# Optimization experiments

Hardware: AMD Instinct MI355X
Metric: run time of the kernel (lower is better)

## Reference

```python
import jax, jax.numpy as jnp
import numpy as np
import math

B, S, D = 16, 1024, 2048  # batch, seq_len, feats_size; LSTM hidden H = D
H = D

def setup_inputs() -> dict:
    key = jax.random.key(0)
    ks = jax.random.split(key, 12)
    s = 1.0 / math.sqrt(D)
    return {
        "feats": jax.random.normal(ks[0], (B, S, D), jnp.float32),
        "Wq": jax.random.normal(ks[1], (D, D), jnp.float32) * s,
        "bq": jnp.zeros((D,), jnp.float32),
        "Wk": jax.random.normal(ks[2], (D, D), jnp.float32) * s,
        "bk": jnp.zeros((D,), jnp.float32),
        "Wv": jax.random.normal(ks[3], (D, D), jnp.float32) * s,
        "bv": jnp.zeros((D,), jnp.float32),
        "W_ih": jax.random.normal(ks[4], (4 * H, D), jnp.float32) * s,
        "W_hh": jax.random.normal(ks[5], (4 * H, H), jnp.float32) * s,
        "b_ih": jnp.zeros((4 * H,), jnp.float32),
        "b_hh": jnp.zeros((4 * H,), jnp.float32),
    }

def _lstm(x, W_ih, W_hh, b_ih, b_hh):
    # x: [B, S, D] -> hidden sequence [B, S, H]. torch nn.LSTM gate order i,f,g,o.
    xg = jnp.einsum('bsd,gd->bsg', x, W_ih) + b_ih + b_hh  # [B,S,4H], input part precomputed
    xg = jnp.swapaxes(xg, 0, 1)  # [S,B,4H] for scan over time
    h0 = jnp.zeros((x.shape[0], H), x.dtype)
    c0 = jnp.zeros((x.shape[0], H), x.dtype)
    def step(carry, xt):
        h, c = carry
        gates = xt + h @ W_hh.T  # [B,4H]
        i, f, g, o = jnp.split(gates, 4, axis=-1)
        c = jax.nn.sigmoid(f) * c + jax.nn.sigmoid(i) * jnp.tanh(g)
        h = jax.nn.sigmoid(o) * jnp.tanh(c)
        return (h, c), h
    _, hs = jax.lax.scan(step, (h0, c0), xg)
    return jnp.swapaxes(hs, 0, 1)  # [B,S,H]

def reference(feats, Wq, bq, Wk, bk, Wv, bv, W_ih, W_hh, b_ih, b_hh):
    q = feats @ Wq.T + bq
    k = feats @ Wk.T + bk
    v = feats @ Wv.T + bv
    dot = jnp.einsum('bsd,btd->bst', q, k) / math.sqrt(2048.0)
    w = jax.nn.softmax(dot, axis=-1)
    new_feats = jnp.einsum('bst,btd->bsd', w, v)
    return _lstm(new_feats, W_ih, W_hh, b_ih, b_hh)
```

## Files before the change

### kernel.cpp

```cpp
#include <hip/hip_runtime.h>


typedef unsigned short u16;
typedef unsigned long long u64;
typedef __attribute__((ext_vector_type(8))) __bf16 bf16x8;
typedef __attribute__((ext_vector_type(8))) unsigned short u16x8;
typedef __attribute__((ext_vector_type(4))) float f32x4;

#define DEV static __device__ __forceinline__

DEV u16 f2bf(float f) {
  union { float f; unsigned u; } x; x.f = f;
  return (u16)((x.u + 0x7FFFu + ((x.u >> 16) & 1u)) >> 16);
}
DEV float bf2f(u16 h) {
  union { unsigned u; float f; } x; x.u = (unsigned)h << 16;
  return x.f;
}
DEV void gload_lds16(const void* g, void* l) {
  __builtin_amdgcn_global_load_lds(
      (const __attribute__((address_space(1))) unsigned int*)g,
      (__attribute__((address_space(3))) unsigned int*)l, 16, 0, 0);
}

__global__ __launch_bounds__(256) void k_cvt(const float* __restrict__ in,
                                             u16* __restrict__ out, long n) {
  long i = (((long)blockIdx.x << 8) | threadIdx.x) << 3;
  if (i >= n) return;
  float4 f0 = *(const float4*)(in + i);
  float4 f1 = *(const float4*)(in + i + 4);
  u16x8 p;
  p[0] = f2bf(f0.x); p[1] = f2bf(f0.y); p[2] = f2bf(f0.z); p[3] = f2bf(f0.w);
  p[4] = f2bf(f1.x); p[5] = f2bf(f1.y); p[6] = f2bf(f1.z); p[7] = f2bf(f1.w);
  *(u16x8*)(out + i) = p;
}

__global__ __launch_bounds__(256) void k_addb(const float* __restrict__ a,
                                              const float* __restrict__ b,
                                              float* __restrict__ o, int n) {
  int i = blockIdx.x * 256 + threadIdx.x;
  if (i < n) o[i] = a[i] + b[i];
}

template<int OBF>
__global__ __launch_bounds__(256) void k_gemm_nt(
    const u16* __restrict__ A, const u16* __restrict__ B, void* __restrict__ Cv,
    const float* __restrict__ bias, float scale, int M, int N, int K,
    long sA, long sB, long sC) {
  __shared__ __attribute__((aligned(16))) u16 As[4096];
  __shared__ __attribute__((aligned(16))) u16 Bs[4096];
  const int tid = threadIdx.x;
  const int lane = tid & 63;
  const int wm = ((tid >> 7) & 1) * 64;
  const int wn = ((tid >> 6) & 1) * 64;
  const int gx = gridDim.x;
  int lin = blockIdx.y * gx + blockIdx.x;
  const int nwg = gx * gridDim.y;
  if ((nwg & 7) == 0) lin = (lin & 7) * (nwg >> 3) + (lin >> 3);
  const long bm = (long)(lin / gx) << 7;
  const long bn = (long)(lin % gx) << 7;
  const u16* Ab = A + (long)blockIdx.z * sA;
  const u16* Bb = B + (long)blockIdx.z * sB;
  const int srow = tid >> 2, scol = (tid & 3) << 3;
  const u16* ga0 = Ab + (bm + srow) * (long)K + scol;
  const u16* gb0 = Bb + (bn + srow) * (long)K + scol;
  const long k64 = (long)K << 6;
  char* lA = (char*)As + tid * 16;
  char* lB = (char*)Bs + tid * 16;
  f32x4 acc[4][4] = {};
  const int fr = lane & 15, fk = (lane >> 4) << 3;
  for (int kt = 0; kt < K; kt += 32) {
    gload_lds16(ga0 + kt, lA);
    gload_lds16(ga0 + k64 + kt, lA + 4096);
    gload_lds16(gb0 + kt, lB);
    gload_lds16(gb0 + k64 + kt, lB + 4096);
    __syncthreads();
    bf16x8 av[4], bv[4];
#pragma unroll
    for (int x = 0; x < 4; ++x) {
      av[x] = *(const bf16x8*)&As[(wm + x * 16 + fr) * 32 + fk];
      bv[x] = *(const bf16x8*)&Bs[(wn + x * 16 + fr) * 32 + fk];
    }
#pragma unroll
    for (int i = 0; i < 4; ++i)
#pragma unroll
      for (int j = 0; j < 4; ++j)
        acc[i][j] = __builtin_amdgcn_mfma_f32_16x16x32_bf16(av[i], bv[j], acc[i][j], 0, 0, 0);
    __syncthreads();
  }
  const long cb = (long)blockIdx.z * sC;
#pragma unroll
  for (int j = 0; j < 4; ++j) {
    const long col = bn + wn + j * 16 + fr;
    const float bb = bias ? bias[col] : 0.f;
#pragma unroll
    for (int i = 0; i < 4; ++i) {
      const long r0 = bm + wm + i * 16 + ((lane >> 4) << 2);
#pragma unroll
      for (int r = 0; r < 4; ++r) {
        const float v = acc[i][j][r] * scale + bb;
        const long off = cb + (r0 + r) * (long)N + col;
        if (OBF) ((u16*)Cv)[off] = f2bf(v);
        else     ((float*)Cv)[off] = v;
      }
    }
  }
}

__global__ __launch_bounds__(256) void k_softmax(const float* __restrict__ S,
                                                 u16* __restrict__ P) {
  __shared__ float red[8];
  const long row = blockIdx.x;
  const float* sr = S + (row << 10);
  const int t = threadIdx.x, lane = t & 63, w = t >> 6;
  float v0 = sr[t], v1 = sr[t + 256], v2 = sr[t + 512], v3 = sr[t + 768];
  float m = fmaxf(fmaxf(v0, v1), fmaxf(v2, v3));
#pragma unroll
  for (int o = 32; o; o >>= 1) m = fmaxf(m, __shfl_xor(m, o));
  if (lane == 0) red[w] = m;
  __syncthreads();
  m = fmaxf(fmaxf(red[0], red[1]), fmaxf(red[2], red[3]));
  v0 = __expf(v0 - m); v1 = __expf(v1 - m); v2 = __expf(v2 - m); v3 = __expf(v3 - m);
  float s = v0 + v1 + v2 + v3;
#pragma unroll
  for (int o = 32; o; o >>= 1) s += __shfl_xor(s, o);
  if (lane == 0) red[4 + w] = s;
  __syncthreads();
  s = red[4] + red[5] + red[6] + red[7];
  const float rs = 1.f / s;
  u16* pr = P + (row << 10);
  pr[t] = f2bf(v0 * rs); pr[t + 256] = f2bf(v1 * rs);
  pr[t + 512] = f2bf(v2 * rs); pr[t + 768] = f2bf(v3 * rs);
}

__global__ __launch_bounds__(256) void k_transpose(const u16* __restrict__ V,
                                                   u16* __restrict__ VT) {
  __shared__ __attribute__((aligned(16))) u16 tile[64][80];
  const long b = blockIdx.z;
  const long t0 = (long)blockIdx.y << 6, d0 = (long)blockIdx.x << 6;
  const int r = threadIdx.x >> 3, c8 = (threadIdx.x & 7) << 3;
  const u16* src = V + ((b << 10) + t0) * 2048 + d0;
#pragma unroll
  for (int p = 0; p < 2; ++p) {
    const int rr = r + p * 32;
    *(u16x8*)&tile[rr][c8] = *(const u16x8*)(src + (long)rr * 2048 + c8);
  }
  __syncthreads();
  u16* dst = VT + ((b << 11) + d0) * 1024 + t0;
#pragma unroll
  for (int p = 0; p < 2; ++p) {
    const int dr = r + p * 32;
    u16x8 pk;
#pragma unroll
    for (int q = 0; q < 8; ++q) pk[q] = tile[c8 + q][dr];
    *(u16x8*)(dst + (long)dr * 1024 + c8) = pk;
  }
}

DEV bf16x8 wread(const char* wlds, int nrow, int k) {
  int byte = (nrow << 12) + (k << 1);
  byte ^= (nrow & 7) << 4;
  return *(const bf16x8*)(wlds + byte);
}
DEV float sigm(float x) { return 1.f / (1.f + __expf(-x)); }
DEV float tanh_fast(float x) { return 1.f - 2.f / (1.f + __expf(2.f * x)); }

__global__ __launch_bounds__(256, 1) void k_lstm(
    const u16* __restrict__ xg, const u16* __restrict__ whh,
    u16* __restrict__ hbuf, float* __restrict__ out,
    unsigned* __restrict__ flg) {
  extern __shared__ char smem[];
  char* wlds = smem;
  float* red = (float*)(smem + 131072);
  const int tid = threadIdx.x, lane = tid & 63, wave = tid >> 6;
  const int j0 = blockIdx.x << 4;
  const int am = lane & 15, ak = (lane >> 4) << 3;
  const int bb = tid >> 4, jj = tid & 15;

  for (int it = 0; it < 32; ++it) {
    const long grow = ((long)(it >> 4) << 11) + j0 + (it & 15);
    const u16* src = whh + grow * 2048 + (tid << 3);
    int byte = (it << 12) + (tid << 4);
    byte ^= (it & 7) << 4;
    *(bf16x8*)(wlds + byte) = *(const bf16x8*)src;
  }
  bf16x8 wf[2][16];
#pragma unroll
  for (int g2 = 0; g2 < 2; ++g2)
#pragma unroll
    for (int ks = 0; ks < 16; ++ks)
      wf[g2][ks] = *(const bf16x8*)(whh + ((long)((2 + g2) << 11) + j0 + am) * 2048 +
                                    (wave << 9) + (ks << 5) + ak);
  __syncthreads();

  float c = 0.f;
  unsigned* const myflag = flg + (((wave << 5) + (lane & 31)) << 2);
  u16 xv[4];
#pragma unroll
  for (int g = 0; g < 4; ++g)
    xv[g] = xg[((long)bb << 10) * 8192 + (g << 11) + j0 + jj];

  for (int t = 0; t < 1024; ++t) {
    const int par = t & 1;
    unsigned dep = 0;
    if (t) {
      const unsigned tgt = (unsigned)t;
      unsigned v = tgt;
      for (;;) {
        if (lane < 32)
          v = __hip_atomic_load(myflag, __ATOMIC_RELAXED, __HIP_MEMORY_SCOPE_AGENT);
        if (__all(v >= tgt)) break;
        __builtin_amdgcn_s_sleep(1);
      }
      dep = v >> 20;
    }
    asm volatile("" : "+v"(dep)::);

    const u64* hq = (const u64*)(hbuf + ((par ^ 1) << 15) + am * 2048 +
                                 (wave << 9) + ak) + dep;
    f32x4 a0 = {0.f, 0.f, 0.f, 0.f}, a1 = a0, a2 = a0, a3 = a0;
#pragma unroll
    for (int ks = 0; ks < 16; ++ks) {
      union { u64 q[2]; bf16x8 v; } u;
      u.q[0] = __hip_atomic_load(hq + (ks << 3),     __ATOMIC_RELAXED, __HIP_MEMORY_SCOPE_AGENT);
      u.q[1] = __hip_atomic_load(hq + (ks << 3) + 1, __ATOMIC_RELAXED, __HIP_MEMORY_SCOPE_AGENT);
      const int k = (wave << 9) + (ks << 5) + ak;
      a0 = __builtin_amdgcn_mfma_f32_16x16x32_bf16(u.v, wread(wlds, am, k),      a0, 0, 0, 0);
      a1 = __builtin_amdgcn_mfma_f32_16x16x32_bf16(u.v, wread(wlds, am + 16, k), a1, 0, 0, 0);
      a2 = __builtin_amdgcn_mfma_f32_16x16x32_bf16(u.v, wf[0][ks], a2, 0, 0, 0);
      a3 = __builtin_amdgcn_mfma_f32_16x16x32_bf16(u.v, wf[1][ks], a3, 0, 0, 0);
    }
    {
      float* rw = red + (wave << 10);
      const int mrow = (lane >> 4) << 2;
#pragma unroll
      for (int r = 0; r < 4; ++r) {
        rw[(mrow + r) * 64 + am]      = a0[r];
        rw[(mrow + r) * 64 + 16 + am] = a1[r];
        rw[(mrow + r) * 64 + 32 + am] = a2[r];
        rw[(mrow + r) * 64 + 48 + am] = a3[r];
      }
    }
    __syncthreads();
    float g4[4];
#pragma unroll
    for (int g = 0; g < 4; ++g) {
      const int n = (bb << 6) + (g << 4) + jj;
      g4[g] = red[n] + red[1024 + n] + red[2048 + n] + red[3072 + n] + bf2f(xv[g]);
    }
    const float gi = sigm(g4[0]);
    const float gf = sigm(g4[1]);
    const float gg = tanh_fast(g4[2]);
    const float go = sigm(g4[3]);
    c = gf * c + gi * gg;
    const float h = go * tanh_fast(c);
    {
      const unsigned hb = (unsigned)f2bf(h);
      const unsigned p1 = (unsigned)__shfl_xor((int)hb, 1);
      const unsigned w2 = (hb & 0xFFFFu) | (p1 << 16);
      const unsigned p2 = (unsigned)__shfl_xor((int)w2, 2);
      if ((jj & 3) == 0) {
        const u64 hw = (u64)w2 | ((u64)p2 << 32);
        u16* dst = hbuf + (par << 15) + (bb << 11) + j0 + jj;
        __hip_atomic_store((u64*)dst, hw, __ATOMIC_RELAXED, __HIP_MEMORY_SCOPE_AGENT);
      }
    }
    asm volatile("s_waitcnt vmcnt(0)" ::: "memory");
    __syncthreads();
    if (tid == 0)
      __hip_atomic_store(flg + (blockIdx.x << 2), (unsigned)(t + 1),
                         __ATOMIC_RELAXED, __HIP_MEMORY_SCOPE_AGENT);
    out[(((long)(bb << 10) + t) << 11) + j0 + jj] = h;
    {
      const int tn = (t + 1 < 1024) ? t + 1 : 0;
#pragma unroll
      for (int g = 0; g < 4; ++g)
        xv[g] = xg[((long)((bb << 10) + tn)) * 8192 + (g << 11) + j0 + jj];
    }
    asm volatile("" ::: "memory");
  }
}

extern "C" void kernel_launch(void* const* d_in, const int* in_sizes, int n_in,
                              void* d_out, int out_size, void* d_ws, size_t ws_size,
                              hipStream_t stream) {
  const float* feats = (const float*)d_in[0];
  const float* Wq = (const float*)d_in[1];
  const float* bq = (const float*)d_in[2];
  const float* Wk = (const float*)d_in[3];
  const float* bk = (const float*)d_in[4];
  const float* Wv = (const float*)d_in[5];
  const float* bv = (const float*)d_in[6];
  const float* Wih = (const float*)d_in[7];
  const float* Whh = (const float*)d_in[8];
  const float* bih = (const float*)d_in[9];
  const float* bhh = (const float*)d_in[10];
  float* out = (float*)d_out;
  char* ws = (char*)d_ws;

  u16* feats16 = (u16*)(ws + 0L);
  u16* q16     = (u16*)(ws + 67108864L);
  u16* k16     = (u16*)(ws + 134217728L);
  u16* v16     = (u16*)(ws + 201326592L);
  u16* vT16    = feats16;
  u16* P16     = q16;
  u16* xg16    = (u16*)(ws + 0L);
  u16* nf16    = (u16*)(ws + 268435456L);
  u16* wq16    = (u16*)(ws + 335544320L);
  u16* wk16    = (u16*)(ws + 343932928L);
  u16* wv16    = (u16*)(ws + 352321536L);
  u16* wih16   = (u16*)(ws + 360710144L);
  u16* whh16   = (u16*)(ws + 394264576L);
  float* biassum = (float*)(ws + 427819008L);
  u16* hbuf    = (u16*)(ws + 427851776L);
  unsigned* flg = (unsigned*)(ws + 427982848L);
  float* scoresf = (float*)d_out;

  k_cvt<<<16384, 256, 0, stream>>>(feats, feats16, 33554432L);
  k_cvt<<<2048, 256, 0, stream>>>(Wq, wq16, 4194304L);
  k_cvt<<<2048, 256, 0, stream>>>(Wk, wk16, 4194304L);
  k_cvt<<<2048, 256, 0, stream>>>(Wv, wv16, 4194304L);
  k_cvt<<<8192, 256, 0, stream>>>(Wih, wih16, 16777216L);
  k_cvt<<<8192, 256, 0, stream>>>(Whh, whh16, 16777216L);
  k_addb<<<32, 256, 0, stream>>>(bih, bhh, biassum, 8192);

  k_gemm_nt<1><<<dim3(16, 128, 1), 256, 0, stream>>>(feats16, wq16, q16, bq, 1.f, 16384, 2048, 2048, 0, 0, 0);
  k_gemm_nt<1><<<dim3(16, 128, 1), 256, 0, stream>>>(feats16, wk16, k16, bk, 1.f, 16384, 2048, 2048, 0, 0, 0);
  k_gemm_nt<1><<<dim3(16, 128, 1), 256, 0, stream>>>(feats16, wv16, v16, bv, 1.f, 16384, 2048, 2048, 0, 0, 0);
  k_gemm_nt<0><<<dim3(8, 8, 16), 256, 0, stream>>>(q16, k16, scoresf, nullptr, 0.022097086912079608f,
                                                   1024, 1024, 2048, 2097152, 2097152, 1048576);
  k_softmax<<<16384, 256, 0, stream>>>(scoresf, P16);
  k_transpose<<<dim3(32, 16, 16), 256, 0, stream>>>(v16, vT16);
  k_gemm_nt<1><<<dim3(16, 8, 16), 256, 0, stream>>>(P16, vT16, nf16, nullptr, 1.f,
                                                    1024, 2048, 1024, 1048576, 2097152, 2097152);
  k_gemm_nt<1><<<dim3(64, 128, 1), 256, 0, stream>>>(nf16, wih16, xg16, biassum, 1.f, 16384, 8192, 2048, 0, 0, 0);

  hipMemsetAsync(ws + 427851776L, 0, 131072 + 4096, stream);
  const int dynlds = 131072 + 16384;
  (void)hipFuncSetAttribute((const void*)k_lstm, hipFuncAttributeMaxDynamicSharedMemorySize, dynlds);
  void* kargs[] = {(void*)&xg16, (void*)&whh16, (void*)&hbuf, (void*)&out, (void*)&flg};
  hipError_t ce = hipLaunchCooperativeKernel((const void*)k_lstm, dim3(128), dim3(256),
                                             kargs, dynlds, stream);
  if (ce != hipSuccess) {
    k_lstm<<<dim3(128), dim3(256), dynlds, stream>>>(xg16, whh16, hbuf, out, flg);
  }
}
```

Before: 8.339 ms.

## Tag each h value with its timestep to replace per-block flag synchronization

The LSTM recurrence now stores each bf16 hidden value together with a 16-bit step tag in a 32-bit word, so consumers poll the h data directly until every tag matches the expected step. This removes the separate flag store, the vmcnt wait plus barrier before publishing, and the extra flag-polling round trip. In exchange the h buffer doubles in size, each poll rereads all 64 words, and unpacking adds ALU work. The 16-bit tag stays unambiguous because there are only 1024 steps.

```diff
diff --git a/kernel.cpp b/kernel.cpp
--- a/kernel.cpp
+++ b/kernel.cpp
@@ -2,6 +2,7 @@
 
 
 typedef unsigned short u16;
+typedef unsigned int u32;
 typedef unsigned long long u64;
 typedef __attribute__((ext_vector_type(8))) __bf16 bf16x8;
 typedef __attribute__((ext_vector_type(8))) unsigned short u16x8;
@@ -167,8 +168,7 @@
 
 __global__ __launch_bounds__(256, 1) void k_lstm(
     const u16* __restrict__ xg, const u16* __restrict__ whh,
-    u16* __restrict__ hbuf, float* __restrict__ out,
-    unsigned* __restrict__ flg) {
+    u32* __restrict__ hbuf, float* __restrict__ out) {
   extern __shared__ char smem[];
   char* wlds = smem;
   float* red = (float*)(smem + 131072);
@@ -194,41 +194,48 @@
   __syncthreads();
 
   float c = 0.f;
-  unsigned* const myflag = flg + (((wave << 5) + (lane & 31)) << 2);
   u16 xv[4];
 #pragma unroll
   for (int g = 0; g < 4; ++g)
     xv[g] = xg[((long)bb << 10) * 8192 + (g << 11) + j0 + jj];
 
+  const u64* const hb64 = (const u64*)hbuf;
+
   for (int t = 0; t < 1024; ++t) {
     const int par = t & 1;
-    unsigned dep = 0;
-    if (t) {
-      const unsigned tgt = (unsigned)t;
-      unsigned v = tgt;
-      for (;;) {
-        if (lane < 32)
-          v = __hip_atomic_load(myflag, __ATOMIC_RELAXED, __HIP_MEMORY_SCOPE_AGENT);
-        if (__all(v >= tgt)) break;
-        __builtin_amdgcn_s_sleep(1);
+    const u64* hq = hb64 + ((long)(par ^ 1) << 14) + (am << 10) + (wave << 8) +
+                    ((lane >> 4) << 2);
+    const u64 expect = (u64)(u32)t | ((u64)(u32)t << 32);
+    u64 hv[64];
+    for (;;) {
+#pragma unroll
+      for (int ks = 0; ks < 16; ++ks)
+#pragma unroll
+        for (int i = 0; i < 4; ++i)
+          hv[(ks << 2) | i] = __hip_atomic_load(hq + (ks << 4) + i,
+                                                __ATOMIC_RELAXED, __HIP_MEMORY_SCOPE_AGENT);
+      u64 acc = 0;
+#pragma unroll
+      for (int x = 0; x < 64; ++x)
+        acc |= (hv[x] ^ expect) & 0x0000FFFF0000FFFFULL;
+      if (__all(acc == 0)) break;
+      __builtin_amdgcn_s_sleep(2);
+    }
+    f32x4 a0 = {0.f, 0.f, 0.f, 0.f}, a1 = a0, a2 = a0, a3 = a0;
+#pragma unroll
+    for (int ks = 0; ks < 16; ++ks) {
+      union { u32 w[4]; bf16x8 v; } frag;
+#pragma unroll
+      for (int i = 0; i < 4; ++i) {
+        const u64 q = hv[(ks << 2) | i];
+        const u32 lo = (u32)q, hi = (u32)(q >> 32);
+        frag.w[i] = (lo >> 16) | (hi & 0xFFFF0000u);
       }
-      dep = v >> 20;
-    }
-    asm volatile("" : "+v"(dep)::);
-
-    const u64* hq = (const u64*)(hbuf + ((par ^ 1) << 15) + am * 2048 +
-                                 (wave << 9) + ak) + dep;
-    f32x4 a0 = {0.f, 0.f, 0.f, 0.f}, a1 = a0, a2 = a0, a3 = a0;
-#pragma unroll
-    for (int ks = 0; ks < 16; ++ks) {
-      union { u64 q[2]; bf16x8 v; } u;
-      u.q[0] = __hip_atomic_load(hq + (ks << 3),     __ATOMIC_RELAXED, __HIP_MEMORY_SCOPE_AGENT);
-      u.q[1] = __hip_atomic_load(hq + (ks << 3) + 1, __ATOMIC_RELAXED, __HIP_MEMORY_SCOPE_AGENT);
       const int k = (wave << 9) + (ks << 5) + ak;
-      a0 = __builtin_amdgcn_mfma_f32_16x16x32_bf16(u.v, wread(wlds, am, k),      a0, 0, 0, 0);
-      a1 = __builtin_amdgcn_mfma_f32_16x16x32_bf16(u.v, wread(wlds, am + 16, k), a1, 0, 0, 0);
-      a2 = __builtin_amdgcn_mfma_f32_16x16x32_bf16(u.v, wf[0][ks], a2, 0, 0, 0);
-      a3 = __builtin_amdgcn_mfma_f32_16x16x32_bf16(u.v, wf[1][ks], a3, 0, 0, 0);
+      a0 = __builtin_amdgcn_mfma_f32_16x16x32_bf16(frag.v, wread(wlds, am, k),      a0, 0, 0, 0);
+      a1 = __builtin_amdgcn_mfma_f32_16x16x32_bf16(frag.v, wread(wlds, am + 16, k), a1, 0, 0, 0);
+      a2 = __builtin_amdgcn_mfma_f32_16x16x32_bf16(frag.v, wf[0][ks], a2, 0, 0, 0);
+      a3 = __builtin_amdgcn_mfma_f32_16x16x32_bf16(frag.v, wf[1][ks], a3, 0, 0, 0);
     }
     {
       float* rw = red + (wave << 10);
@@ -255,21 +262,10 @@
     c = gf * c + gi * gg;
     const float h = go * tanh_fast(c);
     {
-      const unsigned hb = (unsigned)f2bf(h);
-      const unsigned p1 = (unsigned)__shfl_xor((int)hb, 1);
-      const unsigned w2 = (hb & 0xFFFFu) | (p1 << 16);
-      const unsigned p2 = (unsigned)__shfl_xor((int)w2, 2);
-      if ((jj & 3) == 0) {
-        const u64 hw = (u64)w2 | ((u64)p2 << 32);
-        u16* dst = hbuf + (par << 15) + (bb << 11) + j0 + jj;
-        __hip_atomic_store((u64*)dst, hw, __ATOMIC_RELAXED, __HIP_MEMORY_SCOPE_AGENT);
-      }
-    }
-    asm volatile("s_waitcnt vmcnt(0)" ::: "memory");
-    __syncthreads();
-    if (tid == 0)
-      __hip_atomic_store(flg + (blockIdx.x << 2), (unsigned)(t + 1),
+      const u32 hw = ((u32)f2bf(h) << 16) | (u32)(t + 1);
+      __hip_atomic_store(hbuf + ((long)par << 15) + (bb << 11) + j0 + jj, hw,
                          __ATOMIC_RELAXED, __HIP_MEMORY_SCOPE_AGENT);
+    }
     out[(((long)(bb << 10) + t) << 11) + j0 + jj] = h;
     {
       const int tn = (t + 1 < 1024) ? t + 1 : 0;
@@ -278,6 +274,7 @@
         xv[g] = xg[((long)((bb << 10) + tn)) * 8192 + (g << 11) + j0 + jj];
     }
     asm volatile("" ::: "memory");
+    __syncthreads();
   }
 }
 
@@ -312,8 +309,7 @@
   u16* wih16   = (u16*)(ws + 360710144L);
   u16* whh16   = (u16*)(ws + 394264576L);
   float* biassum = (float*)(ws + 427819008L);
-  u16* hbuf    = (u16*)(ws + 427851776L);
-  unsigned* flg = (unsigned*)(ws + 427982848L);
+  u32* hbuf    = (u32*)(ws + 427851776L);
   float* scoresf = (float*)d_out;
 
   k_cvt<<<16384, 256, 0, stream>>>(feats, feats16, 33554432L);
@@ -335,13 +331,13 @@
                                                     1024, 2048, 1024, 1048576, 2097152, 2097152);
   k_gemm_nt<1><<<dim3(64, 128, 1), 256, 0, stream>>>(nf16, wih16, xg16, biassum, 1.f, 16384, 8192, 2048, 0, 0, 0);
 
-  hipMemsetAsync(ws + 427851776L, 0, 131072 + 4096, stream);
+  hipMemsetAsync(ws + 427851776L, 0, 262144, stream);
   const int dynlds = 131072 + 16384;
   (void)hipFuncSetAttribute((const void*)k_lstm, hipFuncAttributeMaxDynamicSharedMemorySize, dynlds);
-  void* kargs[] = {(void*)&xg16, (void*)&whh16, (void*)&hbuf, (void*)&out, (void*)&flg};
+  void* kargs[] = {(void*)&xg16, (void*)&whh16, (void*)&hbuf, (void*)&out};
   hipError_t ce = hipLaunchCooperativeKernel((const void*)k_lstm, dim3(128), dim3(256),
                                              kargs, dynlds, stream);
   if (ce != hipSuccess) {
-    k_lstm<<<dim3(128), dim3(256), dynlds, stream>>>(xg16, whh16, hbuf, out, flg);
-  }
-}
+    k_lstm<<<dim3(128), dim3(256), dynlds, stream>>>(xg16, whh16, hbuf, out);
+  }
+}
```

Result: slower. 16.59 ms (+98.9%).
